# Performance work log

Measured on AMD Instinct MI355X. Metric: run time of the kernel, lower is better.

Reference implementation:

```python
import jax, jax.numpy as jnp
import numpy as np

B, H, W, C = 32, 64, 64, 192
HEADS, WS, SS = 6, 8, 4
N = WS * WS                      # tokens per window = 64
NW = (H // WS) * (W // WS)       # 64 windows
HD = C // HEADS                  # head dim 32
SCALE = HD ** -0.5
HID = 4 * C                      # mlp hidden 768


def _rel_index(ws):
    coords = np.stack(np.meshgrid(np.arange(ws), np.arange(ws), indexing='ij'))
    flat = coords.reshape(2, -1)                       # (2, N)
    rel = (flat[:, :, None] - flat[:, None, :]).transpose(1, 2, 0)  # (N, N, 2)
    rel[..., 0] += ws - 1
    rel[..., 1] += ws - 1
    rel[..., 0] *= 2 * ws - 1
    return jnp.asarray(rel.sum(-1))                    # (N, N) int


def _attn_mask(Hh, Ww, ws, ss):
    img = np.zeros((Hh, Ww))
    cnt = 0
    for hs in (slice(0, -ws), slice(-ws, -ss), slice(-ss, None)):
        for wsl in (slice(0, -ws), slice(-ws, -ss), slice(-ss, None)):
            img[hs, wsl] = cnt
            cnt += 1
    win = img.reshape(Hh // ws, ws, Ww // ws, ws).transpose(0, 2, 1, 3).reshape(-1, ws * ws)
    m = win[:, None, :] - win[:, :, None]              # (nW, N, N)
    return jnp.asarray(np.where(m != 0, -100.0, 0.0).astype(np.float32))


REL_IDX = _rel_index(WS)
MASK = _attn_mask(H, W, WS, SS)


def _ln(x, g, b, eps=1e-5):
    mu = x.mean(-1, keepdims=True)
    var = ((x - mu) ** 2).mean(-1, keepdims=True)
    return (x - mu) * jax.lax.rsqrt(var + eps) * g + b


def setup_inputs() -> dict:
    key = jax.random.key(0)
    ks = jax.random.split(key, 6)
    return {
        'x': jax.random.normal(ks[0], (B, H * W, C), jnp.float32),
        'norm1_g': jnp.ones((C,), jnp.float32),
        'norm1_b': jnp.zeros((C,), jnp.float32),
        'qkv_w': 0.02 * jax.random.normal(ks[1], (C, 3 * C), jnp.float32),
        'qkv_b': jnp.zeros((3 * C,), jnp.float32),
        'rpb_table': 0.02 * jax.random.normal(ks[2], ((2 * WS - 1) ** 2, HEADS), jnp.float32),
        'proj_w': 0.02 * jax.random.normal(ks[3], (C, C), jnp.float32),
        'proj_b': jnp.zeros((C,), jnp.float32),
        'norm2_g': jnp.ones((C,), jnp.float32),
        'norm2_b': jnp.zeros((C,), jnp.float32),
        'fc1_w': 0.02 * jax.random.normal(ks[4], (C, HID), jnp.float32),
        'fc1_b': jnp.zeros((HID,), jnp.float32),
        'fc2_w': 0.02 * jax.random.normal(ks[5], (HID, C), jnp.float32),
        'fc2_b': jnp.zeros((C,), jnp.float32),
    }


def reference(x, norm1_g, norm1_b, qkv_w, qkv_b, rpb_table, proj_w, proj_b,
              norm2_g, norm2_b, fc1_w, fc1_b, fc2_w, fc2_b):
    shortcut = x
    h = _ln(x, norm1_g, norm1_b).reshape(B, H, W, C)
    # cyclic shift
    h = jnp.roll(h, (-SS, -SS), axis=(1, 2))
    # window partition -> (B*nW, N, C)
    hw = h.reshape(B, H // WS, WS, W // WS, WS, C).transpose(0, 1, 3, 2, 4, 5).reshape(B * NW, N, C)
    qkv = (hw @ qkv_w + qkv_b).reshape(B * NW, N, 3, HEADS, HD).transpose(2, 0, 3, 1, 4)
    q, k, v = qkv[0] * SCALE, qkv[1], qkv[2]           # (B*nW, heads, N, HD)
    attn = jnp.einsum('bhnd,bhmd->bhnm', q, k)          # (B*nW, heads, N, N)
    bias = rpb_table[REL_IDX].transpose(2, 0, 1)        # (heads, N, N)
    attn = attn + bias[None]
    attn = attn.reshape(B, NW, HEADS, N, N) + MASK[None, :, None]
    attn = jax.nn.softmax(attn.reshape(B * NW, HEADS, N, N), axis=-1)
    o = jnp.einsum('bhnm,bhmd->bhnd', attn, v).transpose(0, 2, 1, 3).reshape(B * NW, N, C)
    o = o @ proj_w + proj_b
    # window reverse + reverse shift
    o = o.reshape(B, H // WS, W // WS, WS, WS, C).transpose(0, 1, 3, 2, 4, 5).reshape(B, H, W, C)
    o = jnp.roll(o, (SS, SS), axis=(1, 2)).reshape(B, H * W, C)
    x = shortcut + o
    m = _ln(x, norm2_g, norm2_b)
    m = jax.nn.gelu(m @ fc1_w + fc1_b, approximate=False)
    return x + (m @ fc2_w + fc2_b)
```

## Files before the change

### kernel.cpp

```cpp
#include <hip/hip_runtime.h>
#include <math.h>

typedef float f32x4 __attribute__((ext_vector_type(4)));
typedef short short8 __attribute__((ext_vector_type(8)));
typedef unsigned short u16;

#define BB 32
#define CC 192
#define HEADS 6
#define NN 64
#define HID 768
#define NTOK (BB * 64 * 64)
#define SCALE 0.17677669529663687f

#define MFMA(a, b, c) __builtin_amdgcn_mfma_f32_16x16x32_bf16(a, b, c, 0, 0, 0)
#define GLL16(g, l)                                                            \
  __builtin_amdgcn_global_load_lds(                                            \
      (const __attribute__((address_space(1))) void*)(g),                      \
      (__attribute__((address_space(3))) void*)(l), 16, 0, 0)

__device__ __forceinline__ u16 f2bf(float f) {
  union { float f; unsigned int u; } cv;
  cv.f = f;
  unsigned int u = cv.u;
  u += 0x7fffu + ((u >> 16) & 1u);
  return (u16)(u >> 16);
}

__device__ __forceinline__ f32x4 vzero() {
  f32x4 v;
  v[0] = 0.f; v[1] = 0.f; v[2] = 0.f; v[3] = 0.f;
  return v;
}

__device__ __forceinline__ short8 ldsA(const u16* M, int pitch, int r0, int k0, int lane) {
  const int r = r0 + (lane & 15);
  const int cb = ((k0 + ((lane >> 4) << 3)) << 1) ^ ((r & 7) << 4);
  return *(const short8*)(M + r * pitch + (cb >> 1));
}

__device__ __forceinline__ short8 ldsB(const u16* Wb, int col16, int lane) {
  return *(const short8*)(Wb + (((lane >> 4) * 192) + (col16 << 4) + (lane & 15)) * 8);
}

__global__ __launch_bounds__(256) void prep_kernel(
    const float* __restrict__ qkvw, const float* __restrict__ pw,
    const float* __restrict__ w1, const float* __restrict__ w2,
    u16* __restrict__ wqkvT, u16* __restrict__ projT,
    u16* __restrict__ w1T, u16* __restrict__ w2T) {
  const int id = blockIdx.x * 256 + threadIdx.x;
  if (id < 576 * 192) {
    const int e = id & 7;
    const int c = id >> 3;
    const int n = c % 576;
    const int q = c / 576;
    const int kk = q >> 2, kc = q & 3;
    const int k = kk * 32 + kc * 8 + e;
    wqkvT[id] = f2bf(qkvw[k * 576 + n]);
  }
  if (id < 192 * 192) {
    const int e = id & 7;
    const int c = id >> 3;
    const int n = c % 192;
    const int q = c / 192;
    const int kk = q >> 2, kc = q & 3;
    const int k = kk * 32 + kc * 8 + e;
    projT[id] = f2bf(pw[k * 192 + n]);
  }
  if (id < 768 * 192) {
    const int e = id & 7;
    const int c = id >> 3;
    const int n = c % 192;
    const int q = c / 192;
    const int ph = q / 24, r = q % 24;
    const int kk = r >> 2, kc = r & 3;
    const int k = kk * 32 + kc * 8 + e;
    w1T[id] = f2bf(w1[k * 768 + ph * 192 + n]);
  }
  if (id < 192 * 768) {
    const int e = id & 7;
    const int c = id >> 3;
    const int n = c % 192;
    const int q = c / 192;
    const int ph = q / 24, r = q % 24;
    const int kk = r >> 2, kc = r & 3;
    const int k = ph * 192 + kk * 32 + kc * 8 + e;
    w2T[id] = f2bf(w2[k * 192 + n]);
  }
}

__device__ __forceinline__ void stage768_w8(const u16* tbl, int slice,
                                            u16* dst, int w, int lane) {
  const u16* base = tbl + ((size_t)slice * 768) * 8;
  GLL16(base + (w * 64 + lane) * 8, dst + (w * 64) * 8);
  if (w < 4) GLL16(base + (512 + w * 64 + lane) * 8, dst + (512 + w * 64) * 8);
}

__global__ __launch_bounds__(512) void attn_kernel(
    const float* __restrict__ x, const float* __restrict__ n1g,
    const float* __restrict__ n1b, const u16* __restrict__ wqkvT,
    const float* __restrict__ qkvb, const float* __restrict__ rpb,
    u16* __restrict__ hw) {
  __shared__ u16 Xs[64 * 192];
  __shared__ u16 Qs[64 * 192];
  __shared__ u16 Ks[64 * 192];
  __shared__ u16 Vt[192 * 64];
  __shared__ u16 Pb[2][64 * 64];
  __shared__ u16 Wq[4 * 576 * 8];

  const int g = blockIdx.x;
  const int t = threadIdx.x;
  const int w = t >> 6;
  const int lane = t & 63;
  const int b = g >> 6;
  const int wr = (g >> 3) & 7, wc = g & 7;
  u16* win = hw + (size_t)g * (64 * 192);

  {
    const int n = t >> 3;
    const int ch0 = (t & 7) * 24;
    const int sr = ((wr << 3) + (n >> 3) + 4) & 63;
    const int sc = ((wc << 3) + (n & 7) + 4) & 63;
    const float* xp = x + ((size_t)b * 4096 + sr * 64 + sc) * 192 + ch0;
    float v[24];
    float s = 0.f, sq = 0.f;
#pragma unroll
    for (int q = 0; q < 6; ++q) {
      const float4 f4 = *(const float4*)(xp + q * 4);
      v[q * 4 + 0] = f4.x; v[q * 4 + 1] = f4.y;
      v[q * 4 + 2] = f4.z; v[q * 4 + 3] = f4.w;
    }
#pragma unroll
    for (int q = 0; q < 24; ++q) { s += v[q]; sq += v[q] * v[q]; }
#pragma unroll
    for (int msk = 1; msk < 8; msk <<= 1) {
      s += __shfl_xor(s, msk);
      sq += __shfl_xor(sq, msk);
    }
    const float mean = s * (1.f / 192.f);
    const float var = sq * (1.f / 192.f) - mean * mean;
    const float rstd = rsqrtf(var + 1e-5f);
#pragma unroll
    for (int q = 0; q < 12; ++q) {
      const int ch = ch0 + q * 2;
      const float a0 = (v[q * 2] - mean) * rstd * n1g[ch] + n1b[ch];
      const float a1 = (v[q * 2 + 1] - mean) * rstd * n1g[ch + 1] + n1b[ch + 1];
      const unsigned int pk = (unsigned int)f2bf(a0) | ((unsigned int)f2bf(a1) << 16);
      const int cb = (ch << 1) ^ ((n & 7) << 4);
      *(unsigned int*)&Xs[n * 192 + (cb >> 1)] = pk;
    }
  }

  const int ntbeg = (w < 4) ? w * 5 : 20 + (w - 4) * 4;
  const int ntcnt = (w < 4) ? 5 : 4;
  f32x4 acc[5][4];
#pragma unroll
  for (int p = 0; p < 5; ++p)
#pragma unroll
    for (int m = 0; m < 4; ++m) acc[p][m] = vzero();

  for (int kk = 0; kk < 6; ++kk) {
    {
      const u16* src = wqkvT + ((size_t)kk * 2304) * 8;
#pragma unroll
      for (int j = 0; j < 4; ++j) {
        const int cb0 = (j * 8 + w) * 64;
        GLL16(src + (cb0 + lane) * 8, Wq + cb0 * 8);
      }
      if (w < 4) {
        const int cb0 = (32 + w) * 64;
        GLL16(src + (cb0 + lane) * 8, Wq + cb0 * 8);
      }
    }
    __syncthreads();
    short8 a[4];
#pragma unroll
    for (int m = 0; m < 4; ++m) a[m] = ldsA(Xs, 192, m << 4, kk << 5, lane);
#pragma unroll
    for (int p = 0; p < 5; ++p) {
      int nt = ntbeg + p;
      if (nt > 35) nt = 35;
      const short8 bfr = *(const short8*)(
          Wq + (((lane >> 4) * 576) + (nt << 4) + (lane & 15)) * 8);
#pragma unroll
      for (int m = 0; m < 4; ++m) acc[p][m] = MFMA(a[m], bfr, acc[p][m]);
    }
    __syncthreads();
  }

#pragma unroll
  for (int p = 0; p < 5; ++p) {
    if (p < ntcnt) {
      const int cg = ((ntbeg + p) << 4) + (lane & 15);
      const float bias = qkvb[cg];
#pragma unroll
      for (int m = 0; m < 4; ++m) {
#pragma unroll
        for (int i = 0; i < 4; ++i) {
          const int r = (m << 4) + ((lane >> 4) << 2) + i;
          const float val = acc[p][m][i] + bias;
          if (cg < 192) {
            const int cb = (cg << 1) ^ ((r & 7) << 4);
            Qs[r * 192 + (cb >> 1)] = f2bf(val * SCALE);
          } else if (cg < 384) {
            const int cb = ((cg - 192) << 1) ^ ((r & 7) << 4);
            Ks[r * 192 + (cb >> 1)] = f2bf(val);
          } else {
            const int vc = cg - 384;
            const int cb = (r << 1) ^ ((vc & 7) << 4);
            Vt[vc * 64 + (cb >> 1)] = f2bf(val);
          }
        }
      }
    }
  }
  __syncthreads();

  const int s = w >> 2;
  const int mt = w & 3;
  u16* P = Pb[s];
  const int cbase = lane & 15;
  for (int hh = 0; hh < 3; ++hh) {
    const int h = s * 3 + hh;
    const short8 aq = ldsA(Qs, 192, mt << 4, h << 5, lane);
    f32x4 d[4];
#pragma unroll
    for (int kb = 0; kb < 4; ++kb) {
      const short8 bk = ldsA(Ks, 192, kb << 4, h << 5, lane);
      d[kb] = MFMA(aq, bk, vzero());
      const int c = (kb << 4) + cbase;
      const int i2 = c >> 3, j2 = c & 7;
      const int gr2 = (wr << 3) + i2, gc2 = (wc << 3) + j2;
      const int lab2 = (gr2 < 56 ? 0 : (gr2 < 60 ? 1 : 2)) * 3 +
                       (gc2 < 56 ? 0 : (gc2 < 60 ? 1 : 2));
#pragma unroll
      for (int i = 0; i < 4; ++i) {
        const int r = (mt << 4) + ((lane >> 4) << 2) + i;
        const int i1 = r >> 3, j1 = r & 7;
        const int gr1 = (wr << 3) + i1, gc1 = (wc << 3) + j1;
        const int lab1 = (gr1 < 56 ? 0 : (gr1 < 60 ? 1 : 2)) * 3 +
                         (gc1 < 56 ? 0 : (gc1 < 60 ? 1 : 2));
        float v = d[kb][i] + rpb[((i1 - i2 + 7) * 15 + (j1 - j2 + 7)) * HEADS + h];
        if (lab1 != lab2) v -= 100.f;
        d[kb][i] = v;
      }
    }
    float mx[4], sum[4];
#pragma unroll
    for (int i = 0; i < 4; ++i) {
      mx[i] = fmaxf(fmaxf(d[0][i], d[1][i]), fmaxf(d[2][i], d[3][i]));
    }
#pragma unroll
    for (int msk = 1; msk < 16; msk <<= 1) {
#pragma unroll
      for (int i = 0; i < 4; ++i) mx[i] = fmaxf(mx[i], __shfl_xor(mx[i], msk));
    }
#pragma unroll
    for (int i = 0; i < 4; ++i) sum[i] = 0.f;
#pragma unroll
    for (int kb = 0; kb < 4; ++kb) {
#pragma unroll
      for (int i = 0; i < 4; ++i) {
        const float e = __expf(d[kb][i] - mx[i]);
        d[kb][i] = e;
        sum[i] += e;
      }
    }
#pragma unroll
    for (int msk = 1; msk < 16; msk <<= 1) {
#pragma unroll
      for (int i = 0; i < 4; ++i) sum[i] += __shfl_xor(sum[i], msk);
    }
#pragma unroll
    for (int kb = 0; kb < 4; ++kb) {
      const int c = (kb << 4) + cbase;
#pragma unroll
      for (int i = 0; i < 4; ++i) {
        const int r = (mt << 4) + ((lane >> 4) << 2) + i;
        const int cb = (c << 1) ^ ((r & 7) << 4);
        P[r * 64 + (cb >> 1)] = f2bf(d[kb][i] / sum[i]);
      }
    }
#pragma unroll
    for (int nb = 0; nb < 2; ++nb) {
      f32x4 o = vzero();
#pragma unroll
      for (int ks = 0; ks < 2; ++ks) {
        const short8 ap = ldsA(P, 64, mt << 4, ks << 5, lane);
        const short8 bv = ldsA(Vt, 64, (h << 5) + (nb << 4), ks << 5, lane);
        o = MFMA(ap, bv, o);
      }
      const int c = (h << 5) + (nb << 4) + (lane & 15);
#pragma unroll
      for (int i = 0; i < 4; ++i) {
        const int r = (mt << 4) + ((lane >> 4) << 2) + i;
        win[r * 192 + c] = f2bf(o[i]);
      }
    }
  }
}

__global__ __launch_bounds__(256) void proj_kernel(
    const u16* __restrict__ hw, const u16* __restrict__ projT,
    const float* __restrict__ pb, const float* __restrict__ x,
    float* __restrict__ out) {
  __shared__ u16 Os[64 * 192];
  __shared__ u16 Wp[2][768 * 8];
  const int g = blockIdx.x;
  const int t = threadIdx.x;
  const int w = t >> 6;
  const int lane = t & 63;
  const int b_ = g >> 6;
  const int wr = (g >> 3) & 7, wc = g & 7;
  const u16* win = hw + (size_t)g * (64 * 192);
#pragma unroll
  for (int u = 0; u < 6; ++u) {
    const int d = (t * 6 + u) << 4;
    const int row = d / 384;
    const int cb = d - row * 384;
    const short8 v = *(const short8*)((const char*)win + d);
    *(short8*)((char*)Os + row * 384 + (cb ^ ((row & 7) << 4))) = v;
  }
#pragma unroll
  for (int j = 0; j < 3; ++j) {
    const int cb0 = (j * 4 + w) * 64;
    GLL16(projT + (cb0 + lane) * 8, Wp[0] + cb0 * 8);
  }
  int cur = 0;
  f32x4 acc[12];
#pragma unroll
  for (int q = 0; q < 12; ++q) acc[q] = vzero();
  for (int kk = 0; kk < 6; ++kk) {
    __syncthreads();
    if (kk < 5) {
      const u16* src = projT + ((size_t)(kk + 1) * 768) * 8;
#pragma unroll
      for (int j = 0; j < 3; ++j) {
        const int cb0 = (j * 4 + w) * 64;
        GLL16(src + (cb0 + lane) * 8, Wp[cur ^ 1] + cb0 * 8);
      }
    }
    const short8 a = ldsA(Os, 192, w << 4, kk << 5, lane);
#pragma unroll
    for (int q = 0; q < 12; ++q) acc[q] = MFMA(a, ldsB(Wp[cur], q, lane), acc[q]);
    cur ^= 1;
  }
#pragma unroll
  for (int q = 0; q < 12; ++q) {
    const int col = (q << 4) + (lane & 15);
    const float bias = pb[col];
#pragma unroll
    for (int i = 0; i < 4; ++i) {
      const int r = (w << 4) + ((lane >> 4) << 2) + i;
      const int dr = ((wr << 3) + (r >> 3) + 4) & 63;
      const int dc = ((wc << 3) + (r & 7) + 4) & 63;
      const size_t dst = ((size_t)b_ * 4096 + dr * 64 + dc) * 192 + col;
      out[dst] = x[dst] + acc[q][i] + bias;
    }
  }
}

__global__ __launch_bounds__(512, 4) void mlp_kernel(
    float* __restrict__ out, const float* __restrict__ g2,
    const float* __restrict__ bn2, const u16* __restrict__ w1T,
    const float* __restrict__ b1, const u16* __restrict__ w2T,
    const float* __restrict__ bo) {
  __shared__ u16 Xn[64 * 192];
  __shared__ u16 Hs[64 * 192];
  __shared__ u16 Wb[2][768 * 8];
  const size_t T0 = (size_t)blockIdx.x * 64;
  const int t = threadIdx.x;
  const int w = t >> 6;
  const int lane = t & 63;
  const int mt = w & 3;
  const int half = w >> 2;

  {
    const int tok = t >> 3;
    const int ch0 = (t & 7) * 24;
    const float* xp = out + (T0 + tok) * 192 + ch0;
    float v[24];
    float s = 0.f, sq = 0.f;
#pragma unroll
    for (int q = 0; q < 6; ++q) {
      const float4 f4 = *(const float4*)(xp + q * 4);
      v[q * 4 + 0] = f4.x; v[q * 4 + 1] = f4.y;
      v[q * 4 + 2] = f4.z; v[q * 4 + 3] = f4.w;
    }
#pragma unroll
    for (int q = 0; q < 24; ++q) { s += v[q]; sq += v[q] * v[q]; }
#pragma unroll
    for (int msk = 1; msk < 8; msk <<= 1) {
      s += __shfl_xor(s, msk);
      sq += __shfl_xor(sq, msk);
    }
    const float mean = s * (1.f / 192.f);
    const float var = sq * (1.f / 192.f) - mean * mean;
    const float rstd = rsqrtf(var + 1e-5f);
#pragma unroll
    for (int q = 0; q < 12; ++q) {
      const int ch = ch0 + q * 2;
      const float a0 = (v[q * 2] - mean) * rstd * g2[ch] + bn2[ch];
      const float a1 = (v[q * 2 + 1] - mean) * rstd * g2[ch + 1] + bn2[ch + 1];
      const unsigned int pk = (unsigned int)f2bf(a0) | ((unsigned int)f2bf(a1) << 16);
      const int cb = (ch << 1) ^ ((tok & 7) << 4);
      *(unsigned int*)&Xn[tok * 192 + (cb >> 1)] = pk;
    }
  }

  f32x4 acc2[6];
#pragma unroll
  for (int p = 0; p < 6; ++p) acc2[p] = vzero();
  int cur = 0;

  stage768_w8(w1T, 0, Wb[0], w, lane);

  for (int ph = 0; ph < 4; ++ph) {
    f32x4 acc1[6];
#pragma unroll
    for (int p = 0; p < 6; ++p) acc1[p] = vzero();
#pragma unroll
    for (int kk = 0; kk < 6; ++kk) {
      __syncthreads();
      if (kk < 5) stage768_w8(w1T, ph * 6 + kk + 1, Wb[cur ^ 1], w, lane);
      else        stage768_w8(w2T, ph * 6, Wb[cur ^ 1], w, lane);
      const short8 a = ldsA(Xn, 192, mt << 4, kk << 5, lane);
#pragma unroll
      for (int p = 0; p < 6; ++p)
        acc1[p] = MFMA(a, ldsB(Wb[cur], half * 6 + p, lane), acc1[p]);
      cur ^= 1;
    }
#pragma unroll
    for (int p = 0; p < 6; ++p) {
      const int lcol = ((half * 6 + p) << 4) + (lane & 15);
      const float bias = b1[ph * 192 + lcol];
#pragma unroll
      for (int i = 0; i < 4; ++i) {
        const int r = (mt << 4) + ((lane >> 4) << 2) + i;
        const float hv = acc1[p][i] + bias;
        const float ge = 0.5f * hv * (1.0f + erff(hv * 0.70710678118654752f));
        const int cb = (lcol << 1) ^ ((r & 7) << 4);
        Hs[r * 192 + (cb >> 1)] = f2bf(ge);
      }
    }
#pragma unroll
    for (int kk = 0; kk < 6; ++kk) {
      __syncthreads();
      if (kk < 5)      stage768_w8(w2T, ph * 6 + kk + 1, Wb[cur ^ 1], w, lane);
      else if (ph < 3) stage768_w8(w1T, (ph + 1) * 6, Wb[cur ^ 1], w, lane);
      const short8 a = ldsA(Hs, 192, mt << 4, kk << 5, lane);
#pragma unroll
      for (int p = 0; p < 6; ++p)
        acc2[p] = MFMA(a, ldsB(Wb[cur], half * 6 + p, lane), acc2[p]);
      cur ^= 1;
    }
  }

#pragma unroll
  for (int p = 0; p < 6; ++p) {
    const int col = ((half * 6 + p) << 4) + (lane & 15);
    const float bias = bo[col];
#pragma unroll
    for (int i = 0; i < 4; ++i) {
      const int r = (mt << 4) + ((lane >> 4) << 2) + i;
      float* op = out + (T0 + r) * 192 + col;
      *op = *op + acc2[p][i] + bias;
    }
  }
}

extern "C" void kernel_launch(void* const* d_in, const int* in_sizes, int n_in,
                              void* d_out, int out_size, void* d_ws, size_t ws_size,
                              hipStream_t stream) {
  const float* x    = (const float*)d_in[0];
  const float* n1g  = (const float*)d_in[1];
  const float* n1b  = (const float*)d_in[2];
  const float* qkvw = (const float*)d_in[3];
  const float* qkvb = (const float*)d_in[4];
  const float* rpb  = (const float*)d_in[5];
  const float* pw   = (const float*)d_in[6];
  const float* pb   = (const float*)d_in[7];
  const float* n2g  = (const float*)d_in[8];
  const float* n2b  = (const float*)d_in[9];
  const float* w1   = (const float*)d_in[10];
  const float* b1   = (const float*)d_in[11];
  const float* w2   = (const float*)d_in[12];
  const float* b2   = (const float*)d_in[13];
  float* out = (float*)d_out;

  u16* hw    = (u16*)d_ws;
  u16* wqkvT = hw + (size_t)131072 * 192;
  u16* projT = wqkvT + 576 * 192;
  u16* w1T   = projT + 192 * 192;
  u16* w2T   = w1T + 768 * 192;

  prep_kernel<<<576, 256, 0, stream>>>(qkvw, pw, w1, w2, wqkvT, projT, w1T, w2T);
  attn_kernel<<<2048, 512, 0, stream>>>(x, n1g, n1b, wqkvT, qkvb, rpb, hw);
  proj_kernel<<<2048, 256, 0, stream>>>(hw, projT, pb, x, out);
  mlp_kernel<<<2048, 512, 0, stream>>>(out, n2g, n2b, w1T, b1, w2T, b2);
}
```

Before: 432.7 us.

## Stage epilogues through LDS for vectorized stores and use fast GELU approximation

The proj and MLP epilogues now write accumulators into a swizzled fp32 LDS tile, which aliases the input buffers. Each thread then reads whole token rows, so the residual add and global stores become coalesced float4 accesses instead of scattered scalar ones. The attention kernel stages its output tile in LDS before a vectorized copy to global memory. Exact erff GELU is replaced by the Abramowitz-Stegun polynomial with a fast reciprocal and exp, trading some accuracy (around 1e-7 absolute error) for fewer ALU instructions, at the cost of extra syncs and LDS round trips.

```diff
diff --git a/kernel.cpp b/kernel.cpp
--- a/kernel.cpp
+++ b/kernel.cpp
@@ -31,6 +31,21 @@
   f32x4 v;
   v[0] = 0.f; v[1] = 0.f; v[2] = 0.f; v[3] = 0.f;
   return v;
+}
+
+__device__ __forceinline__ float gelu_f(float x) {
+  const float z = 0.70710678118654752f * x;
+  const float az = fabsf(z);
+  const float tt = __builtin_amdgcn_rcpf(1.0f + 0.3275911f * az);
+  const float e = __expf(-az * az);
+  float poly = 1.061405429f;
+  poly = poly * tt - 1.453152027f;
+  poly = poly * tt + 1.421413741f;
+  poly = poly * tt - 0.284496736f;
+  poly = poly * tt + 0.254829592f;
+  float er = 1.0f - poly * tt * e;
+  er = z < 0.f ? -er : er;
+  return 0.5f * x * (1.0f + er);
 }
 
 __device__ __forceinline__ short8 ldsA(const u16* M, int pitch, int r0, int k0, int lane) {
@@ -294,9 +309,15 @@
 #pragma unroll
       for (int i = 0; i < 4; ++i) {
         const int r = (mt << 4) + ((lane >> 4) << 2) + i;
-        win[r * 192 + c] = f2bf(o[i]);
-      }
-    }
+        Xs[r * 192 + c] = f2bf(o[i]);
+      }
+    }
+  }
+  __syncthreads();
+#pragma unroll
+  for (int u = 0; u < 6; ++u) {
+    const int d = t * 6 + u;
+    *(short8*)((char*)win + (d << 4)) = *(const short8*)((const char*)Xs + (d << 4));
   }
 }
 
@@ -304,8 +325,11 @@
     const u16* __restrict__ hw, const u16* __restrict__ projT,
     const float* __restrict__ pb, const float* __restrict__ x,
     float* __restrict__ out) {
-  __shared__ u16 Os[64 * 192];
-  __shared__ u16 Wp[2][768 * 8];
+  __shared__ __align__(16) char sbuf[49152];
+  u16* Os = (u16*)sbuf;
+  u16* Wp0 = (u16*)(sbuf + 24576);
+  u16* Wp1 = (u16*)(sbuf + 36864);
+  float* Ef = (float*)sbuf;
   const int g = blockIdx.x;
   const int t = threadIdx.x;
   const int w = t >> 6;
@@ -324,7 +348,7 @@
 #pragma unroll
   for (int j = 0; j < 3; ++j) {
     const int cb0 = (j * 4 + w) * 64;
-    GLL16(projT + (cb0 + lane) * 8, Wp[0] + cb0 * 8);
+    GLL16(projT + (cb0 + lane) * 8, Wp0 + cb0 * 8);
   }
   int cur = 0;
   f32x4 acc[12];
@@ -334,17 +358,20 @@
     __syncthreads();
     if (kk < 5) {
       const u16* src = projT + ((size_t)(kk + 1) * 768) * 8;
+      u16* dstW = cur ? Wp0 : Wp1;
 #pragma unroll
       for (int j = 0; j < 3; ++j) {
         const int cb0 = (j * 4 + w) * 64;
-        GLL16(src + (cb0 + lane) * 8, Wp[cur ^ 1] + cb0 * 8);
+        GLL16(src + (cb0 + lane) * 8, dstW + cb0 * 8);
       }
     }
     const short8 a = ldsA(Os, 192, w << 4, kk << 5, lane);
-#pragma unroll
-    for (int q = 0; q < 12; ++q) acc[q] = MFMA(a, ldsB(Wp[cur], q, lane), acc[q]);
+    const u16* curW = cur ? Wp1 : Wp0;
+#pragma unroll
+    for (int q = 0; q < 12; ++q) acc[q] = MFMA(a, ldsB(curW, q, lane), acc[q]);
     cur ^= 1;
   }
+  __syncthreads();
 #pragma unroll
   for (int q = 0; q < 12; ++q) {
     const int col = (q << 4) + (lane & 15);
@@ -352,10 +379,27 @@
 #pragma unroll
     for (int i = 0; i < 4; ++i) {
       const int r = (w << 4) + ((lane >> 4) << 2) + i;
-      const int dr = ((wr << 3) + (r >> 3) + 4) & 63;
-      const int dc = ((wc << 3) + (r & 7) + 4) & 63;
-      const size_t dst = ((size_t)b_ * 4096 + dr * 64 + dc) * 192 + col;
-      out[dst] = x[dst] + acc[q][i] + bias;
+      Ef[r * 192 + (col ^ ((r & 7) << 2))] = acc[q][i] + bias;
+    }
+  }
+  __syncthreads();
+  {
+    const int tok = t >> 2;
+    const int c0 = (t & 3) * 48;
+    const int dr = ((wr << 3) + (tok >> 3) + 4) & 63;
+    const int dc = ((wc << 3) + (tok & 7) + 4) & 63;
+    const size_t dst = ((size_t)b_ * 4096 + dr * 64 + dc) * 192 + c0;
+    const float* erow = Ef + tok * 192;
+    const int swz = (tok & 7) << 2;
+#pragma unroll
+    for (int j = 0; j < 12; ++j) {
+      const float4 ov = *(const float4*)(erow + ((c0 + j * 4) ^ swz));
+      float4 xv = *(const float4*)(x + dst + j * 4);
+      xv.x += ov.x;
+      xv.y += ov.y;
+      xv.z += ov.z;
+      xv.w += ov.w;
+      *(float4*)(out + dst + j * 4) = xv;
     }
   }
 }
@@ -365,9 +409,12 @@
     const float* __restrict__ bn2, const u16* __restrict__ w1T,
     const float* __restrict__ b1, const u16* __restrict__ w2T,
     const float* __restrict__ bo) {
-  __shared__ u16 Xn[64 * 192];
-  __shared__ u16 Hs[64 * 192];
-  __shared__ u16 Wb[2][768 * 8];
+  __shared__ __align__(16) char sbuf[73728];
+  u16* Xn = (u16*)sbuf;
+  u16* Hs = (u16*)(sbuf + 24576);
+  u16* Wb0 = (u16*)(sbuf + 49152);
+  u16* Wb1 = (u16*)(sbuf + 61440);
+  float* Ef = (float*)sbuf;
   const size_t T0 = (size_t)blockIdx.x * 64;
   const int t = threadIdx.x;
   const int w = t >> 6;
@@ -413,7 +460,7 @@
   for (int p = 0; p < 6; ++p) acc2[p] = vzero();
   int cur = 0;
 
-  stage768_w8(w1T, 0, Wb[0], w, lane);
+  stage768_w8(w1T, 0, Wb0, w, lane);
 
   for (int ph = 0; ph < 4; ++ph) {
     f32x4 acc1[6];
@@ -422,12 +469,14 @@
 #pragma unroll
     for (int kk = 0; kk < 6; ++kk) {
       __syncthreads();
-      if (kk < 5) stage768_w8(w1T, ph * 6 + kk + 1, Wb[cur ^ 1], w, lane);
-      else        stage768_w8(w2T, ph * 6, Wb[cur ^ 1], w, lane);
+      u16* nxtW = cur ? Wb0 : Wb1;
+      if (kk < 5) stage768_w8(w1T, ph * 6 + kk + 1, nxtW, w, lane);
+      else        stage768_w8(w2T, ph * 6, nxtW, w, lane);
       const short8 a = ldsA(Xn, 192, mt << 4, kk << 5, lane);
+      const u16* curW = cur ? Wb1 : Wb0;
 #pragma unroll
       for (int p = 0; p < 6; ++p)
-        acc1[p] = MFMA(a, ldsB(Wb[cur], half * 6 + p, lane), acc1[p]);
+        acc1[p] = MFMA(a, ldsB(curW, half * 6 + p, lane), acc1[p]);
       cur ^= 1;
     }
 #pragma unroll
@@ -438,7 +487,7 @@
       for (int i = 0; i < 4; ++i) {
         const int r = (mt << 4) + ((lane >> 4) << 2) + i;
         const float hv = acc1[p][i] + bias;
-        const float ge = 0.5f * hv * (1.0f + erff(hv * 0.70710678118654752f));
+        const float ge = gelu_f(hv);
         const int cb = (lcol << 1) ^ ((r & 7) << 4);
         Hs[r * 192 + (cb >> 1)] = f2bf(ge);
       }
@@ -446,16 +495,19 @@
 #pragma unroll
     for (int kk = 0; kk < 6; ++kk) {
       __syncthreads();
-      if (kk < 5)      stage768_w8(w2T, ph * 6 + kk + 1, Wb[cur ^ 1], w, lane);
-      else if (ph < 3) stage768_w8(w1T, (ph + 1) * 6, Wb[cur ^ 1], w, lane);
+      u16* nxtW = cur ? Wb0 : Wb1;
+      if (kk < 5)      stage768_w8(w2T, ph * 6 + kk + 1, nxtW, w, lane);
+      else if (ph < 3) stage768_w8(w1T, (ph + 1) * 6, nxtW, w, lane);
       const short8 a = ldsA(Hs, 192, mt << 4, kk << 5, lane);
+      const u16* curW = cur ? Wb1 : Wb0;
 #pragma unroll
       for (int p = 0; p < 6; ++p)
-        acc2[p] = MFMA(a, ldsB(Wb[cur], half * 6 + p, lane), acc2[p]);
+        acc2[p] = MFMA(a, ldsB(curW, half * 6 + p, lane), acc2[p]);
       cur ^= 1;
     }
   }
 
+  __syncthreads();
 #pragma unroll
   for (int p = 0; p < 6; ++p) {
     const int col = ((half * 6 + p) << 4) + (lane & 15);
@@ -463,8 +515,25 @@
 #pragma unroll
     for (int i = 0; i < 4; ++i) {
       const int r = (mt << 4) + ((lane >> 4) << 2) + i;
-      float* op = out + (T0 + r) * 192 + col;
-      *op = *op + acc2[p][i] + bias;
+      Ef[r * 192 + (col ^ ((r & 7) << 2))] = acc2[p][i] + bias;
+    }
+  }
+  __syncthreads();
+  {
+    const int tok = t >> 3;
+    const int ch0 = (t & 7) * 24;
+    float* op = out + (T0 + tok) * 192 + ch0;
+    const float* erow = Ef + tok * 192;
+    const int swz = (tok & 7) << 2;
+#pragma unroll
+    for (int q = 0; q < 6; ++q) {
+      const float4 ov = *(const float4*)(erow + ((ch0 + q * 4) ^ swz));
+      float4 xv = *(const float4*)(op + q * 4);
+      xv.x += ov.x;
+      xv.y += ov.y;
+      xv.z += ov.z;
+      xv.w += ov.w;
+      *(float4*)(op + q * 4) = xv;
     }
   }
 }
```

Result: no change. 435.4 us (+0.6%).
